# Performance work log

Hardware: AMD Instinct MI355X
Metric: run time of the kernel (lower is better)

## Reference

```python
import jax, jax.numpy as jnp
import numpy as np

BN_EPS = 1e-5
NUM_SUBSET = 3


def conv1x1(x, w, b):
    # x: [N, C, T, V], w: [O, C], b: [O]  (1x1 Conv2d)
    return jnp.einsum('nctv,oc->notv', x, w) + b[:, None, None]


def setup_inputs() -> dict:
    key = jax.random.key(0)
    ks = jax.random.split(key, 8)
    N, C, T, V = 64, 64, 300, 25
    IC = 16  # inter_c = out_channels // coff_embedding
    O = 64
    inp = {
        'x': jax.random.normal(ks[0], (N, C, T, V), dtype=jnp.float32),
        'A': jax.random.uniform(ks[1], (NUM_SUBSET, V, V), dtype=jnp.float32),
        'graph_attn': jnp.ones((NUM_SUBSET, V, V), dtype=jnp.float32),
        'g_w': jax.random.normal(ks[2], (NUM_SUBSET, O, C), dtype=jnp.float32) * 0.05,
        'g_b': jnp.zeros((NUM_SUBSET, O), dtype=jnp.float32),
        'a_w': jax.random.normal(ks[3], (NUM_SUBSET, IC, C), dtype=jnp.float32) * 0.05,
        'a_b': jnp.zeros((NUM_SUBSET, IC), dtype=jnp.float32),
        'b_w': jax.random.normal(ks[4], (NUM_SUBSET, IC, C), dtype=jnp.float32) * 0.05,
        'b_b': jnp.zeros((NUM_SUBSET, IC), dtype=jnp.float32),
        'bn_gamma': jnp.ones((O,), dtype=jnp.float32),
        'bn_beta': jnp.zeros((O,), dtype=jnp.float32),
        'bn_mean': jnp.zeros((O,), dtype=jnp.float32),
        'bn_var': jnp.ones((O,), dtype=jnp.float32),
    }
    return inp


def reference(x, A, graph_attn, g_w, g_b, a_w, a_b, b_w, b_b,
              bn_gamma, bn_beta, bn_mean, bn_var):
    N, C, T, V = x.shape
    IC = a_w.shape[1]
    A_tot = A + graph_attn  # [3, V, V]
    x_flat = x.reshape(N, C * T, V)
    hidden = None
    for i in range(NUM_SUBSET):
        # a_conv -> permute(0,3,1,2) -> [N, V, IC*T]
        A1 = conv1x1(x, a_w[i], a_b[i]).transpose(0, 3, 1, 2).reshape(N, V, IC * T)
        # b_conv -> [N, IC*T, V]
        A2 = conv1x1(x, b_w[i], b_b[i]).reshape(N, IC * T, V)
        attn = jax.nn.softmax(jnp.matmul(A1, A2) / (IC * T), axis=-2)  # [N, V, V], softmax over rows
        attn = attn + A_tot[i]
        z = jnp.matmul(x_flat, attn).reshape(N, C, T, V)
        z = conv1x1(z, g_w[i], g_b[i])
        hidden = z if hidden is None else hidden + z
    # BatchNorm2d in eval mode over channel dim
    inv = jax.lax.rsqrt(bn_var + BN_EPS)
    hidden = (hidden - bn_mean[:, None, None]) * (inv * bn_gamma)[:, None, None] + bn_beta[:, None, None]
    # in_channels == out_channels -> identity residual
    hidden = hidden + x
    return jax.nn.relu(hidden)
```

## Files before the change

kernel.cpp:

```cpp
#include <hip/hip_runtime.h>


#define NB 64
#define CB 64
#define TB 300
#define VB 25

typedef unsigned int uint32;
typedef unsigned short ushort16;
typedef __attribute__((ext_vector_type(8))) short short8;
typedef __attribute__((ext_vector_type(4))) float f32x4;
typedef __attribute__((ext_vector_type(16))) float f32x16;

__device__ __forceinline__ ushort16 f2bf(float f) {
    uint32 u = __float_as_uint(f);
    u = u + 0x7FFFu + ((u >> 16) & 1u);
    return (ushort16)(u >> 16);
}
__device__ __forceinline__ float bf2f(ushort16 h) {
    return __uint_as_float(((uint32)h) << 16);
}
__device__ __forceinline__ uint32 packbf2(float a, float b) {
    return (uint32)f2bf(a) | ((uint32)f2bf(b) << 16);
}

__device__ __forceinline__ int xt_swz(int kb, int tv) {
    return ((kb + tv + (tv >> 2)) & 7) << 3;
}

__global__ __launch_bounds__(256) void k1_attn_logits_mfma(
    const float* __restrict__ x, const float* __restrict__ a_w,
    const float* __restrict__ a_b, const float* __restrict__ b_w,
    const float* __restrict__ b_b, float* __restrict__ Mb)
{
    __shared__ ushort16 ws[96 * 64];
    __shared__ ushort16 xT[112 * 64];
    __shared__ ushort16 abT[192 * 64];
    __shared__ float    bias[96];

    const int tid   = threadIdx.x;
    const int n     = blockIdx.x / 25;
    const int chunk = blockIdx.x % 25;
    const float* xn = x + n * (CB * TB * VB);

    for (int idx = tid; idx < 3072; idx += 256) {
        int r = idx >> 5, cp = idx & 31;
        int c = cp * 2;
        float2 v2 = (r < 48) ? *(const float2*)(a_w + r * 64 + c)
                             : *(const float2*)(b_w + (r - 48) * 64 + c);
        *(uint32*)&ws[r * 64 + ((((c >> 3) + r) & 7) << 3) + (c & 7)] =
            packbf2(v2.x, v2.y);
    }
    for (int idx = tid; idx < 96; idx += 256)
        bias[idx] = (idx < 48) ? a_b[idx] : b_b[idx - 48];

    const int w    = tid >> 6;
    const int lane = tid & 63;
    const int l15  = lane & 15;
    const int q    = lane >> 4;
    const int hi   = lane >> 5;
    const int v32  = lane & 31;

    f32x16 acc;
    #pragma unroll
    for (int r = 0; r < 16; ++r) acc[r] = 0.f;
    const f32x4 zf = (f32x4){0.f, 0.f, 0.f, 0.f};

    for (int s = 0; s < 3; ++s) {
        __syncthreads();
        const float* xs0 = xn + (chunk * 12 + s * 4) * 25;
        for (int idx = tid; idx < 1600; idx += 256) {
            int c = idx / 25, j = idx % 25;
            float4 v4 = *(const float4*)(xs0 + c * 7500 + j * 4);
            int tv0 = j * 4;
            #pragma unroll
            for (int e = 0; e < 4; ++e) {
                int tv = tv0 + e;
                float fv = (e == 0) ? v4.x : (e == 1) ? v4.y : (e == 2) ? v4.z : v4.w;
                xT[tv * 64 + xt_swz(c >> 3, tv) + (c & 7)] = f2bf(fv);
            }
        }
        __syncthreads();
        for (int tile = w; tile < 42; tile += 4) {
            int rt = tile / 7, ct = tile % 7;
            int r  = rt * 16 + l15;
            int tv = ct * 16 + l15;
            f32x4 d = zf;
            #pragma unroll
            for (int ss = 0; ss < 2; ++ss) {
                int kb = ss * 4 + q;
                short8 af = *(const short8*)&ws[r * 64 + (((kb + r) & 7) << 3)];
                short8 bf = *(const short8*)&xT[tv * 64 + xt_swz(kb, tv)];
                d = __builtin_amdgcn_mfma_f32_16x16x32_bf16(af, bf, d, 0, 0, 0);
            }
            if (tv < 100) {
                int tl = tv / 25, v = tv % 25;
                int r0 = rt * 16 + q * 4;
                float b0 = bias[r0], b1 = bias[r0 + 1];
                float b2 = bias[r0 + 2], b3 = bias[r0 + 3];
                int kb = tl * 2 + (q >> 1);
                uint32* dst = (uint32*)&abT[(rt * 32 + v) * 64 +
                                            (((kb + v) & 7) << 3) + ((q & 1) << 2)];
                dst[0] = packbf2(d[0] + b0, d[1] + b1);
                dst[1] = packbf2(d[2] + b2, d[3] + b3);
            }
        }
        __syncthreads();
        if (w < 3) {
            #pragma unroll
            for (int tl = 0; tl < 4; ++tl) {
                int kb = tl * 2 + hi;
                short8 af = *(const short8*)&abT[(w * 32 + v32) * 64 +
                                                 (((kb + v32) & 7) << 3)];
                short8 bf = *(const short8*)&abT[((3 + w) * 32 + v32) * 64 +
                                                 (((kb + v32) & 7) << 3)];
                acc = __builtin_amdgcn_mfma_f32_32x32x16_bf16(af, bf, acc, 0, 0, 0);
            }
        }
    }

    if (w < 3 && v32 < 25) {
        const float inv = 1.0f / 4800.0f;
        #pragma unroll
        for (int r = 0; r < 16; ++r) {
            int row = (r & 3) + 8 * (r >> 2) + 4 * hi;
            if (row < 25)
                atomicAdd(Mb + ((w * NB + n) * 25 + row) * 25 + v32, acc[r] * inv);
        }
    }
}

__global__ __launch_bounds__(64) void k2_softmax_prep(
    const float* __restrict__ Mb, const float* __restrict__ A,
    const float* __restrict__ GA, const float* __restrict__ g_w,
    uint32* __restrict__ atT, uint32* __restrict__ gwb)
{
    const int b   = blockIdx.x;
    const int tid = threadIdx.x;
    if (b < 192) {
        __shared__ float Ms[640];
        const int i = b >> 6, n = b & 63;
        const float* src = Mb + b * 625;
        for (int idx = tid; idx < 625; idx += 64) Ms[idx] = src[idx];
        __syncthreads();
        if (tid < 25) {
            const int v2 = tid;
            float e[25], mx = -1e30f;
            #pragma unroll
            for (int v1 = 0; v1 < 25; ++v1) {
                e[v1] = Ms[v1 * 25 + v2];
                mx = fmaxf(mx, e[v1]);
            }
            float s = 0.f;
            #pragma unroll
            for (int v1 = 0; v1 < 25; ++v1) { e[v1] = __expf(e[v1] - mx); s += e[v1]; }
            float invs = 1.0f / s;
            const float* acol = A + i * 625 + v2;
            const float* gcol = GA + i * 625 + v2;
            float wv[25];
            #pragma unroll
            for (int v1 = 0; v1 < 25; ++v1)
                wv[v1] = e[v1] * invs + acol[v1 * 25] + gcol[v1 * 25];
            uint32* row = atT + ((i * 64 + n) * 32 + v2) * 16;
            #pragma unroll
            for (int p = 0; p < 12; ++p) row[p] = packbf2(wv[2 * p], wv[2 * p + 1]);
            row[12] = (uint32)f2bf(wv[24]);
            row[13] = 0u; row[14] = 0u; row[15] = 0u;
        }
    } else {
        int j0 = (b - 192) * 256 + tid * 4;
        #pragma unroll
        for (int u = 0; u < 4; ++u) {
            int j = j0 + u;
            int o = j / 96, kp = j % 96;
            int k0 = 2 * kp, i = k0 >> 6, c = k0 & 63;
            float2 lh = *(const float2*)(g_w + (i * 64 + o) * 64 + c);
            gwb[j] = packbf2(lh.x, lh.y);
        }
    }
}

__global__ __launch_bounds__(256) void k3_out(
    const float* __restrict__ x, const uint32* __restrict__ atT,
    const ushort16* __restrict__ gwb, const float* __restrict__ g_b,
    const float* __restrict__ bn_g, const float* __restrict__ bn_b,
    const float* __restrict__ bn_m, const float* __restrict__ bn_v,
    float* __restrict__ out)
{
    __shared__ ushort16 xs[64 * 168];
    __shared__ uint32  xa[128 * 36];
    __shared__ uint32  ats[3 * 32 * 20];
    __shared__ float   bsc[64], bsh[64];

    const int tid = threadIdx.x;
    const int n  = blockIdx.x / 60;
    const int t0 = (blockIdx.x % 60) * 5;

    for (int idx = tid; idx < 8000; idx += 256) {
        int c = idx / 125, tv = idx % 125;
        int t = tv / 25, v = tv % 25;
        float g = x[((n * 64 + c) * 300 + t0 + t) * 25 + v];
        xs[c * 168 + t * 32 + v] = f2bf(g);
    }
    for (int idx = tid; idx < 64 * 35; idx += 256) {
        int c = idx / 35, r = idx % 35;
        xs[c * 168 + (r / 7) * 32 + 25 + (r % 7)] = (ushort16)0;
    }
    for (int idx = tid; idx < 1536; idx += 256) {
        int row = idx >> 4, d = idx & 15;
        ats[row * 20 + d] = atT[((row >> 5) * 64 + n) * 512 + (row & 31) * 16 + d];
    }
    for (int idx = tid; idx < 64; idx += 256) {
        float sc = bn_g[idx] * rsqrtf(bn_v[idx] + 1e-5f);
        bsc[idx] = sc;
        bsh[idx] = (g_b[idx] + g_b[64 + idx] + g_b[128 + idx] - bn_m[idx]) * sc + bn_b[idx];
    }
    for (int idx = tid; idx < 3 * 36; idx += 256)
        xa[(125 + idx / 36) * 36 + idx % 36] = 0u;

    const int w    = tid >> 6;
    const int lane = tid & 63;
    const int l15  = lane & 15;
    const int q    = lane >> 4;

    short8 gf[6];
    #pragma unroll
    for (int s = 0; s < 6; ++s)
        gf[s] = *(const short8*)(gwb + ((w * 16 + l15) * 192 + s * 32 + q * 8));

    f32x4 acc[8];
    #pragma unroll
    for (int ct = 0; ct < 8; ++ct) acc[ct] = (f32x4){0.f, 0.f, 0.f, 0.f};
    const f32x4 zf = (f32x4){0.f, 0.f, 0.f, 0.f};

    __syncthreads();

    for (int i = 0; i < 3; ++i) {
        if (i) __syncthreads();
        #pragma unroll
        for (int t = 0; t < 5; ++t) {
            short8 ax = *(const short8*)(xs + (w * 16 + l15) * 168 + t * 32 + q * 8);
            #pragma unroll
            for (int vt = 0; vt < 2; ++vt) {
                short8 bt = *(const short8*)((const ushort16*)ats +
                                             (i * 32 + vt * 16 + l15) * 40 + q * 8);
                f32x4 d = __builtin_amdgcn_mfma_f32_16x16x32_bf16(ax, bt, zf, 0, 0, 0);
                int v2 = vt * 16 + l15;
                if (v2 < 25) {
                    int col = t * 25 + v2;
                    int c0  = w * 16 + q * 4;
                    xa[col * 36 + (c0 >> 1)]     = packbf2(d[0], d[1]);
                    xa[col * 36 + (c0 >> 1) + 1] = packbf2(d[2], d[3]);
                }
            }
        }
        __syncthreads();
        #pragma unroll
        for (int ct = 0; ct < 8; ++ct) {
            #pragma unroll
            for (int s = 0; s < 2; ++s) {
                short8 bfrag = *(const short8*)((const ushort16*)xa +
                                                (ct * 16 + l15) * 72 + s * 32 + q * 8);
                acc[ct] = __builtin_amdgcn_mfma_f32_16x16x32_bf16(
                    gf[i * 2 + s], bfrag, acc[ct], 0, 0, 0);
            }
        }
    }

    const int o0 = w * 16 + q * 4;
    #pragma unroll
    for (int ct = 0; ct < 8; ++ct) {
        int col = ct * 16 + l15;
        if (col < 125) {
            int tl = col / 25;
            int v  = col - tl * 25;
            float* ob = out + (n * 64 + o0) * 7500 + t0 * 25 + col;
            #pragma unroll
            for (int r = 0; r < 4; ++r) {
                int o = o0 + r;
                float xv = bf2f(xs[o * 168 + tl * 32 + v]);
                float h = acc[ct][r] * bsc[o] + bsh[o] + xv;
                ob[r * 7500] = fmaxf(h, 0.f);
            }
        }
    }
}

extern "C" void kernel_launch(void* const* d_in, const int* in_sizes, int n_in,
                              void* d_out, int out_size, void* d_ws, size_t ws_size,
                              hipStream_t stream) {
    const float* x    = (const float*)d_in[0];
    const float* A    = (const float*)d_in[1];
    const float* GA   = (const float*)d_in[2];
    const float* g_w  = (const float*)d_in[3];
    const float* g_b  = (const float*)d_in[4];
    const float* a_w  = (const float*)d_in[5];
    const float* a_b  = (const float*)d_in[6];
    const float* b_w  = (const float*)d_in[7];
    const float* b_b  = (const float*)d_in[8];
    const float* bn_g = (const float*)d_in[9];
    const float* bn_b = (const float*)d_in[10];
    const float* bn_m = (const float*)d_in[11];
    const float* bn_v = (const float*)d_in[12];
    float* out = (float*)d_out;

    float*  Mb  = (float*)d_ws;
    uint32* atT = (uint32*)((char*)d_ws + 480000);
    uint32* gwb = (uint32*)((char*)d_ws + 480000 + 393216);

    hipMemsetAsync(d_ws, 0, 480000, stream);
    k1_attn_logits_mfma<<<dim3(1600), dim3(256), 0, stream>>>(x, a_w, a_b, b_w, b_b, Mb);
    k2_softmax_prep<<<dim3(216), dim3(64), 0, stream>>>(Mb, A, GA, g_w, atT, gwb);
    k3_out<<<dim3(3840), dim3(256), 0, stream>>>(x, atT, (const ushort16*)gwb,
                                                 g_b, bn_g, bn_b, bn_m, bn_v, out);
}
```

Before: 373.0 us.

## Restructure attention-logit kernel: prefetch x, hoist weight conversion, use 32x32 MFMA

```diff
diff --git a/kernel.cpp b/kernel.cpp
--- a/kernel.cpp
+++ b/kernel.cpp
@@ -1,4 +1,5 @@
 #include <hip/hip_runtime.h>
+#include <hip/hip_bf16.h>
 
 
 #define NB 64
@@ -13,9 +14,10 @@
 typedef __attribute__((ext_vector_type(16))) float f32x16;
 
 __device__ __forceinline__ ushort16 f2bf(float f) {
-    uint32 u = __float_as_uint(f);
-    u = u + 0x7FFFu + ((u >> 16) & 1u);
-    return (ushort16)(u >> 16);
+    __hip_bfloat16 h = __float2bfloat16(f);
+    ushort16 u;
+    __builtin_memcpy(&u, &h, sizeof(u));
+    return u;
 }
 __device__ __forceinline__ float bf2f(ushort16 h) {
     return __uint_as_float(((uint32)h) << 16);
@@ -24,97 +26,137 @@
     return (uint32)f2bf(a) | ((uint32)f2bf(b) << 16);
 }
 
-__device__ __forceinline__ int xt_swz(int kb, int tv) {
-    return ((kb + tv + (tv >> 2)) & 7) << 3;
-}
-
-__global__ __launch_bounds__(256) void k1_attn_logits_mfma(
-    const float* __restrict__ x, const float* __restrict__ a_w,
-    const float* __restrict__ a_b, const float* __restrict__ b_w,
-    const float* __restrict__ b_b, float* __restrict__ Mb)
+__global__ __launch_bounds__(256) void k0_prep(
+    const float* __restrict__ a_w, const float* __restrict__ b_w,
+    const float* __restrict__ g_w,
+    ushort16* __restrict__ wb2, uint32* __restrict__ gwb)
 {
-    __shared__ ushort16 ws[96 * 64];
-    __shared__ ushort16 xT[112 * 64];
-    __shared__ ushort16 abT[192 * 64];
-    __shared__ float    bias[96];
+    int idx = blockIdx.x * 256 + threadIdx.x;
+    if (idx < 6144) {
+        int kb = idx / 768, rem = idx % 768;
+        int r = rem >> 3, ci = rem & 7;
+        int c = kb * 8 + ci;
+        float v = (r < 48) ? a_w[r * 64 + c] : b_w[(r - 48) * 64 + c];
+        wb2[idx] = f2bf(v);
+    } else if (idx < 12288) {
+        int j = idx - 6144;
+        int o = j / 96, kp = j % 96;
+        int k0 = 2 * kp, i = k0 >> 6, c = k0 & 63;
+        float2 lh = *(const float2*)(g_w + (i * 64 + o) * 64 + c);
+        gwb[j] = packbf2(lh.x, lh.y);
+    }
+}
+
+__global__ __launch_bounds__(256, 4) void k1_attn_logits_mfma(
+    const float* __restrict__ x, const ushort16* __restrict__ wb2,
+    const float* __restrict__ a_b, const float* __restrict__ b_b,
+    float* __restrict__ Mb)
+{
+    __shared__ ushort16 pool[20352];
+    ushort16* xT  = pool;
+    ushort16* abT = pool + 126 * 64;
 
     const int tid   = threadIdx.x;
     const int n     = blockIdx.x / 25;
     const int chunk = blockIdx.x % 25;
     const float* xn = x + n * (CB * TB * VB);
 
-    for (int idx = tid; idx < 3072; idx += 256) {
-        int r = idx >> 5, cp = idx & 31;
-        int c = cp * 2;
-        float2 v2 = (r < 48) ? *(const float2*)(a_w + r * 64 + c)
-                             : *(const float2*)(b_w + (r - 48) * 64 + c);
-        *(uint32*)&ws[r * 64 + ((((c >> 3) + r) & 7) << 3) + (c & 7)] =
-            packbf2(v2.x, v2.y);
-    }
-    for (int idx = tid; idx < 96; idx += 256)
-        bias[idx] = (idx < 48) ? a_b[idx] : b_b[idx - 48];
+    if (tid < 96) {
+        float v = (tid < 48) ? a_b[tid] : b_b[tid - 48];
+        ((float*)(abT + (31 + (tid >> 5) * 32) * 64))[tid & 31] = v;
+    }
 
     const int w    = tid >> 6;
     const int lane = tid & 63;
-    const int l15  = lane & 15;
-    const int q    = lane >> 4;
     const int hi   = lane >> 5;
     const int v32  = lane & 31;
 
-    f32x16 acc;
-    #pragma unroll
-    for (int r = 0; r < 16; ++r) acc[r] = 0.f;
-    const f32x4 zf = (f32x4){0.f, 0.f, 0.f, 0.f};
+    int goff[7], xps[7];
+    #pragma unroll
+    for (int k = 0; k < 7; ++k) {
+        int idx = tid + k * 256;
+        int c = idx / 25, j = idx - c * 25;
+        goff[k] = c * 7500 + j * 4;
+        int sb  = ((c >> 3) + 5 * j) & 7;
+        xps[k]  = ((4 * j) * 64 + (c & 7)) * 8 + sb;
+    }
+    const float* xb0 = xn + chunk * 12 * 25;
+
+    float4 pf[7];
+    #pragma unroll
+    for (int k = 0; k < 7; ++k)
+        if (tid + k * 256 < 1600)
+            pf[k] = *(const float4*)(xb0 + goff[k]);
+
+    const int tv     = w * 32 + v32;
+    const bool avalid = tv < 100;
+    const int tl = tv / 25;
+    const int vv = tv - tl * 25;
+
+    f32x16 accB;
+    #pragma unroll
+    for (int r = 0; r < 16; ++r) accB[r] = 0.f;
 
     for (int s = 0; s < 3; ++s) {
         __syncthreads();
-        const float* xs0 = xn + (chunk * 12 + s * 4) * 25;
-        for (int idx = tid; idx < 1600; idx += 256) {
-            int c = idx / 25, j = idx % 25;
-            float4 v4 = *(const float4*)(xs0 + c * 7500 + j * 4);
-            int tv0 = j * 4;
-            #pragma unroll
-            for (int e = 0; e < 4; ++e) {
-                int tv = tv0 + e;
-                float fv = (e == 0) ? v4.x : (e == 1) ? v4.y : (e == 2) ? v4.z : v4.w;
-                xT[tv * 64 + xt_swz(c >> 3, tv) + (c & 7)] = f2bf(fv);
-            }
+        #pragma unroll
+        for (int k = 0; k < 7; ++k) {
+            if (tid + k * 256 < 1600) {
+                float4 v4 = pf[k];
+                int base = xps[k] >> 3, sb = xps[k] & 7;
+                xT[base + 0 * 64 + (((sb + 0) & 7) << 3)] = f2bf(v4.x);
+                xT[base + 1 * 64 + (((sb + 1) & 7) << 3)] = f2bf(v4.y);
+                xT[base + 2 * 64 + (((sb + 2) & 7) << 3)] = f2bf(v4.z);
+                xT[base + 3 * 64 + (((sb + 3) & 7) << 3)] = f2bf(v4.w);
+            }
+        }
+        if (s < 2) {
+            const float* xbn = xb0 + (s + 1) * 100;
+            #pragma unroll
+            for (int k = 0; k < 7; ++k)
+                if (tid + k * 256 < 1600)
+                    pf[k] = *(const float4*)(xbn + goff[k]);
         }
         __syncthreads();
-        for (int tile = w; tile < 42; tile += 4) {
-            int rt = tile / 7, ct = tile % 7;
-            int r  = rt * 16 + l15;
-            int tv = ct * 16 + l15;
-            f32x4 d = zf;
-            #pragma unroll
-            for (int ss = 0; ss < 2; ++ss) {
-                int kb = ss * 4 + q;
-                short8 af = *(const short8*)&ws[r * 64 + (((kb + r) & 7) << 3)];
-                short8 bf = *(const short8*)&xT[tv * 64 + xt_swz(kb, tv)];
-                d = __builtin_amdgcn_mfma_f32_16x16x32_bf16(af, bf, d, 0, 0, 0);
-            }
-            if (tv < 100) {
-                int tl = tv / 25, v = tv % 25;
-                int r0 = rt * 16 + q * 4;
-                float b0 = bias[r0], b1 = bias[r0 + 1];
-                float b2 = bias[r0 + 2], b3 = bias[r0 + 3];
-                int kb = tl * 2 + (q >> 1);
-                uint32* dst = (uint32*)&abT[(rt * 32 + v) * 64 +
-                                            (((kb + v) & 7) << 3) + ((q & 1) << 2)];
-                dst[0] = packbf2(d[0] + b0, d[1] + b1);
-                dst[1] = packbf2(d[2] + b2, d[3] + b3);
+        #pragma unroll
+        for (int rt = 0; rt < 3; ++rt) {
+            f32x16 d;
+            #pragma unroll
+            for (int r = 0; r < 16; ++r) d[r] = 0.f;
+            #pragma unroll
+            for (int k16 = 0; k16 < 4; ++k16) {
+                int kb = k16 * 2 + hi;
+                short8 af = *(const short8*)(wb2 + (kb * 96 + rt * 32 + v32) * 8);
+                short8 bf = *(const short8*)&xT[tv * 64 +
+                                                (((kb + tv + (tv >> 2)) & 7) << 3)];
+                d = __builtin_amdgcn_mfma_f32_32x32x16_bf16(af, bf, d, 0, 0, 0);
+            }
+            if (avalid) {
+                #pragma unroll
+                for (int a = 0; a < 4; ++a) {
+                    int rowoff = 8 * a + 4 * hi;
+                    int g   = rt * 2 + (rowoff >> 4);
+                    int icb = rowoff & 15;
+                    float4 bq = *(const float4*)(
+                        (const float*)(abT + (31 + rt * 32) * 64) + rowoff);
+                    int kbw = tl * 2 + (icb >> 3);
+                    uint32* dst = (uint32*)&abT[(g * 32 + vv) * 64 +
+                                                (((kbw + vv) & 7) << 3) + (icb & 7)];
+                    dst[0] = packbf2(d[4 * a + 0] + bq.x, d[4 * a + 1] + bq.y);
+                    dst[1] = packbf2(d[4 * a + 2] + bq.z, d[4 * a + 3] + bq.w);
+                }
             }
         }
         __syncthreads();
         if (w < 3) {
             #pragma unroll
-            for (int tl = 0; tl < 4; ++tl) {
-                int kb = tl * 2 + hi;
+            for (int tl2 = 0; tl2 < 4; ++tl2) {
+                int kb = tl2 * 2 + hi;
                 short8 af = *(const short8*)&abT[(w * 32 + v32) * 64 +
                                                  (((kb + v32) & 7) << 3)];
                 short8 bf = *(const short8*)&abT[((3 + w) * 32 + v32) * 64 +
                                                  (((kb + v32) & 7) << 3)];
-                acc = __builtin_amdgcn_mfma_f32_32x32x16_bf16(af, bf, acc, 0, 0, 0);
+                accB = __builtin_amdgcn_mfma_f32_32x32x16_bf16(af, bf, accB, 0, 0, 0);
             }
         }
     }
@@ -125,58 +167,45 @@
         for (int r = 0; r < 16; ++r) {
             int row = (r & 3) + 8 * (r >> 2) + 4 * hi;
             if (row < 25)
-                atomicAdd(Mb + ((w * NB + n) * 25 + row) * 25 + v32, acc[r] * inv);
-        }
-    }
-}
-
-__global__ __launch_bounds__(64) void k2_softmax_prep(
+                atomicAdd(Mb + ((w * NB + n) * 25 + row) * 25 + v32, accB[r] * inv);
+        }
+    }
+}
+
+__global__ __launch_bounds__(128) void k2_softmax(
     const float* __restrict__ Mb, const float* __restrict__ A,
-    const float* __restrict__ GA, const float* __restrict__ g_w,
-    uint32* __restrict__ atT, uint32* __restrict__ gwb)
+    const float* __restrict__ GA, uint32* __restrict__ atT)
 {
+    __shared__ float Ms[640];
     const int b   = blockIdx.x;
     const int tid = threadIdx.x;
-    if (b < 192) {
-        __shared__ float Ms[640];
-        const int i = b >> 6, n = b & 63;
-        const float* src = Mb + b * 625;
-        for (int idx = tid; idx < 625; idx += 64) Ms[idx] = src[idx];
-        __syncthreads();
-        if (tid < 25) {
-            const int v2 = tid;
-            float e[25], mx = -1e30f;
-            #pragma unroll
-            for (int v1 = 0; v1 < 25; ++v1) {
-                e[v1] = Ms[v1 * 25 + v2];
-                mx = fmaxf(mx, e[v1]);
-            }
-            float s = 0.f;
-            #pragma unroll
-            for (int v1 = 0; v1 < 25; ++v1) { e[v1] = __expf(e[v1] - mx); s += e[v1]; }
-            float invs = 1.0f / s;
-            const float* acol = A + i * 625 + v2;
-            const float* gcol = GA + i * 625 + v2;
-            float wv[25];
-            #pragma unroll
-            for (int v1 = 0; v1 < 25; ++v1)
-                wv[v1] = e[v1] * invs + acol[v1 * 25] + gcol[v1 * 25];
-            uint32* row = atT + ((i * 64 + n) * 32 + v2) * 16;
-            #pragma unroll
-            for (int p = 0; p < 12; ++p) row[p] = packbf2(wv[2 * p], wv[2 * p + 1]);
-            row[12] = (uint32)f2bf(wv[24]);
-            row[13] = 0u; row[14] = 0u; row[15] = 0u;
-        }
-    } else {
-        int j0 = (b - 192) * 256 + tid * 4;
-        #pragma unroll
-        for (int u = 0; u < 4; ++u) {
-            int j = j0 + u;
-            int o = j / 96, kp = j % 96;
-            int k0 = 2 * kp, i = k0 >> 6, c = k0 & 63;
-            float2 lh = *(const float2*)(g_w + (i * 64 + o) * 64 + c);
-            gwb[j] = packbf2(lh.x, lh.y);
-        }
+    const int i = b >> 6, n = b & 63;
+    const float* src = Mb + b * 625;
+    for (int idx = tid; idx < 625; idx += 128) Ms[idx] = src[idx];
+    __syncthreads();
+    if (tid < 25) {
+        const int v2 = tid;
+        float e[25], mx = -1e30f;
+        #pragma unroll
+        for (int v1 = 0; v1 < 25; ++v1) {
+            e[v1] = Ms[v1 * 25 + v2];
+            mx = fmaxf(mx, e[v1]);
+        }
+        float s = 0.f;
+        #pragma unroll
+        for (int v1 = 0; v1 < 25; ++v1) { e[v1] = __expf(e[v1] - mx); s += e[v1]; }
+        float invs = 1.0f / s;
+        const float* acol = A + i * 625 + v2;
+        const float* gcol = GA + i * 625 + v2;
+        float wv[25];
+        #pragma unroll
+        for (int v1 = 0; v1 < 25; ++v1)
+            wv[v1] = e[v1] * invs + acol[v1 * 25] + gcol[v1 * 25];
+        uint32* row = atT + ((i * 64 + n) * 32 + v2) * 16;
+        #pragma unroll
+        for (int p = 0; p < 12; ++p) row[p] = packbf2(wv[2 * p], wv[2 * p + 1]);
+        row[12] = (uint32)f2bf(wv[24]);
+        row[13] = 0u; row[14] = 0u; row[15] = 0u;
     }
 }
 
@@ -304,13 +333,15 @@
     const float* bn_v = (const float*)d_in[12];
     float* out = (float*)d_out;
 
-    float*  Mb  = (float*)d_ws;
-    uint32* atT = (uint32*)((char*)d_ws + 480000);
-    uint32* gwb = (uint32*)((char*)d_ws + 480000 + 393216);
+    float*    Mb  = (float*)d_ws;
+    uint32*   atT = (uint32*)((char*)d_ws + 480000);
+    ushort16* wb2 = (ushort16*)((char*)d_ws + 480000);
+    uint32*   gwb = (uint32*)((char*)d_ws + 480000 + 393216);
 
     hipMemsetAsync(d_ws, 0, 480000, stream);
-    k1_attn_logits_mfma<<<dim3(1600), dim3(256), 0, stream>>>(x, a_w, a_b, b_w, b_b, Mb);
-    k2_softmax_prep<<<dim3(216), dim3(64), 0, stream>>>(Mb, A, GA, g_w, atT, gwb);
+    k0_prep<<<dim3(48), dim3(256), 0, stream>>>(a_w, b_w, g_w, wb2, gwb);
+    k1_attn_logits_mfma<<<dim3(1600), dim3(256), 0, stream>>>(x, wb2, a_b, b_b, Mb);
+    k2_softmax<<<dim3(192), dim3(128), 0, stream>>>(Mb, A, GA, atT);
     k3_out<<<dim3(3840), dim3(256), 0, stream>>>(x, atT, (const ushort16*)gwb,
                                                  g_b, bn_g, bn_b, bn_m, bn_v, out);
 }
```

Result: no change. 377.9 us (+1.3%).
